# Kernel optimization log

Measured on AMD Instinct MI355X. Metric: run time of the kernel, lower is better.

## Reference

```python
import jax, jax.numpy as jnp
import numpy as np

B, N, D = 4, 4096, 512
E = 4 * D            # expanded_dim = 2048
TAIL = E // 2        # tail_dim = 1024
HALF = TAIL // 2     # mt_half = 512
HEAD = E - TAIL      # head_dim = 1024
EPS_RMS = 1e-6
EPS_NORM = 1e-12


def setup_inputs() -> dict:
    key = jax.random.key(0)
    k = jax.random.split(key, 6)
    x = jax.random.normal(k[0], (B, N, D), dtype=jnp.float32)
    g = jnp.ones((D,), dtype=jnp.float32)                                   # RMSNorm gain
    W1 = jax.random.normal(k[1], (D, E), dtype=jnp.float32) * 0.02          # Enricher linear
    b1 = jnp.zeros((E,), dtype=jnp.float32)
    V = jax.random.normal(k[2], (N, N), dtype=jnp.float32) * 0.02           # learned positional matrix slice
    bias = jnp.zeros((HALF,), dtype=jnp.float32)                            # contextualizer bias
    Wf = jax.random.normal(k[3], (HEAD + HALF, D), dtype=jnp.float32) * 0.02  # Fuser linear (no bias)
    return {"x": x, "g": g, "W1": W1, "b1": b1, "V": V, "bias": bias, "Wf": Wf}


def reference(x, g, W1, b1, V, bias, Wf):
    # RMSNorm
    xn = x * jax.lax.rsqrt(jnp.mean(jnp.square(x), axis=-1, keepdims=True) + EPS_RMS) * g
    # Enricher: relu(linear)^2
    enriched = jnp.square(jax.nn.relu(xn @ W1 + b1))                        # [B, N, E]
    head = enriched[..., :HEAD]                                             # [B, N, HEAD]
    tail = enriched[..., HEAD:]                                             # [B, N, TAIL]
    # Contextualizer
    x_left = tail[..., :HALF]
    x_right = tail[..., HALF:]
    nrm = jnp.sqrt(jnp.sum(jnp.square(x_right), axis=-1, keepdims=True))
    xr_n = x_right / jnp.maximum(nrm, EPS_NORM)                             # F.normalize, p=2
    cos = jnp.einsum('bnd,bmd->bnm', xr_n, xr_n)                            # [B, N, N] cosine sim
    weighted = V[None, :, :] * cos                                          # elementwise learned V
    ctx = jnp.einsum('bnm,bmd->bnd', weighted, xr_n)                        # chunked-path bmm uses x_right_norm
    ctx = jax.nn.sigmoid(ctx + bias)
    gated = x_left * ctx                                                    # [B, N, HALF]
    # Fuser + residual
    out = jnp.concatenate([head, gated], axis=-1) @ Wf                      # [B, N, D]
    return x + out
```

## Files before the change

### kernel.cpp

```cpp
#include <hip/hip_runtime.h>
#include <stdint.h>

typedef unsigned short u16;
typedef unsigned long long u64;
typedef __attribute__((ext_vector_type(8))) short bf16x8;
typedef __attribute__((ext_vector_type(4))) float f32x4;
typedef __attribute__((ext_vector_type(16))) float f32x16;
typedef __attribute__((ext_vector_type(4))) unsigned int u32x4;
typedef __attribute__((ext_vector_type(4))) unsigned short u16x4;

#define DEV static __device__ __forceinline__

DEV u16 f2bf(float f){
  unsigned u = __builtin_bit_cast(unsigned, f);
  u += 0x7fffu + ((u >> 16) & 1u);
  return (u16)(u >> 16);
}
DEV float bf2f(u16 v){
  unsigned u = ((unsigned)v) << 16;
  return __builtin_bit_cast(float, u);
}

DEV void async_lds16(const void* g, void* l){
  __builtin_amdgcn_global_load_lds(
      (const __attribute__((address_space(1))) unsigned int*)g,
      (__attribute__((address_space(3))) unsigned int*)l, 16, 0, 0);
}

DEV f32x4 mfma16(bf16x8 a, bf16x8 b, f32x4 c){
  return __builtin_amdgcn_mfma_f32_16x16x32_bf16(a, b, c, 0, 0, 0);
}
DEV f32x16 mfma32(bf16x8 a, bf16x8 b, f32x16 c){
  return __builtin_amdgcn_mfma_f32_32x32x16_bf16(a, b, c, 0, 0, 0);
}

__global__ __launch_bounds__(64) void k_rms(const float* __restrict__ x,
                                            const float* __restrict__ g,
                                            u16* __restrict__ xn){
  const int row = blockIdx.x;
  const int l = threadIdx.x;
  const float* xr = x + (size_t)row * 512 + l * 8;
  f32x4 a = *(const f32x4*)xr;
  f32x4 c = *(const f32x4*)(xr + 4);
  float s = a[0]*a[0]+a[1]*a[1]+a[2]*a[2]+a[3]*a[3]
          + c[0]*c[0]+c[1]*c[1]+c[2]*c[2]+c[3]*c[3];
  #pragma unroll
  for (int off = 32; off >= 1; off >>= 1) s += __shfl_xor(s, off);
  float sc = rsqrtf(s * (1.f/512.f) + 1e-6f);
  f32x4 g0 = *(const f32x4*)&g[l*8];
  f32x4 g1 = *(const f32x4*)&g[l*8+4];
  u32x4 o;
  o[0] = (unsigned)f2bf(a[0]*sc*g0[0]) | ((unsigned)f2bf(a[1]*sc*g0[1]) << 16);
  o[1] = (unsigned)f2bf(a[2]*sc*g0[2]) | ((unsigned)f2bf(a[3]*sc*g0[3]) << 16);
  o[2] = (unsigned)f2bf(c[0]*sc*g1[0]) | ((unsigned)f2bf(c[1]*sc*g1[1]) << 16);
  o[3] = (unsigned)f2bf(c[2]*sc*g1[2]) | ((unsigned)f2bf(c[3]*sc*g1[3]) << 16);
  *(u32x4*)&xn[(size_t)row*512 + l*8] = o;
}

__global__ __launch_bounds__(64) void k_norm(const float* __restrict__ xr_in,
                                             u16* __restrict__ xrn){
  const int row = blockIdx.x;
  const int l = threadIdx.x;
  const float* xr = xr_in + (size_t)row * 512 + l * 8;
  f32x4 a = *(const f32x4*)xr;
  f32x4 c = *(const f32x4*)(xr + 4);
  float s = a[0]*a[0]+a[1]*a[1]+a[2]*a[2]+a[3]*a[3]
          + c[0]*c[0]+c[1]*c[1]+c[2]*c[2]+c[3]*c[3];
  #pragma unroll
  for (int off = 32; off >= 1; off >>= 1) s += __shfl_xor(s, off);
  float sc = 1.f / fmaxf(sqrtf(s), 1e-12f);
  u32x4 o;
  o[0] = (unsigned)f2bf(a[0]*sc) | ((unsigned)f2bf(a[1]*sc) << 16);
  o[1] = (unsigned)f2bf(a[2]*sc) | ((unsigned)f2bf(a[3]*sc) << 16);
  o[2] = (unsigned)f2bf(c[0]*sc) | ((unsigned)f2bf(c[1]*sc) << 16);
  o[3] = (unsigned)f2bf(c[2]*sc) | ((unsigned)f2bf(c[3]*sc) << 16);
  *(u32x4*)&xrn[(size_t)row*512 + l*8] = o;
}

__global__ __launch_bounds__(256) void k_castV(const float* __restrict__ V,
                                               u16* __restrict__ Vb){
  size_t i = ((size_t)blockIdx.x * 256 + threadIdx.x) * 8;
  f32x4 a = *(const f32x4*)&V[i];
  f32x4 c = *(const f32x4*)&V[i+4];
  u32x4 o;
  o[0] = (unsigned)f2bf(a[0]) | ((unsigned)f2bf(a[1]) << 16);
  o[1] = (unsigned)f2bf(a[2]) | ((unsigned)f2bf(a[3]) << 16);
  o[2] = (unsigned)f2bf(c[0]) | ((unsigned)f2bf(c[1]) << 16);
  o[3] = (unsigned)f2bf(c[2]) | ((unsigned)f2bf(c[3]) << 16);
  *(u32x4*)&Vb[i] = o;
}

__global__ __launch_bounds__(256) void k_tr32(const float* __restrict__ in,
                                              u16* __restrict__ out, int R, int C){
  __shared__ float tile[32][33];
  const int t = threadIdx.x;
  const int r = t >> 3;
  const int c4 = (t & 7) << 2;
  const int r0 = blockIdx.y << 5, c0 = blockIdx.x << 5;
  f32x4 v = *(const f32x4*)&in[(size_t)(r0 + r) * C + c0 + c4];
  tile[r][c4+0]=v[0]; tile[r][c4+1]=v[1]; tile[r][c4+2]=v[2]; tile[r][c4+3]=v[3];
  __syncthreads();
  u64 o =
      (u64)f2bf(tile[c4+0][r])
    | ((u64)f2bf(tile[c4+1][r]) << 16)
    | ((u64)f2bf(tile[c4+2][r]) << 32)
    | ((u64)f2bf(tile[c4+3][r]) << 48);
  *(u64*)&out[(size_t)(c0 + r) * R + r0 + c4] = o;
}

__global__ __launch_bounds__(256) void k_trb(const u16* __restrict__ in,
                                             u16* __restrict__ out, int R, int C){
  __shared__ u16 tile[32][40];
  const int t = threadIdx.x;
  const int r = t >> 3;
  const int c4 = (t & 7) << 2;
  const size_t bb = (size_t)blockIdx.z * R * C;
  const int r0 = blockIdx.y << 5, c0 = blockIdx.x << 5;
  u64 v = *(const u64*)&in[bb + (size_t)(r0 + r)*C + c0 + c4];
  tile[r][c4+0]=(u16)v; tile[r][c4+1]=(u16)(v>>16);
  tile[r][c4+2]=(u16)(v>>32); tile[r][c4+3]=(u16)(v>>48);
  __syncthreads();
  u64 o =
      (u64)tile[c4+0][r]
    | ((u64)tile[c4+1][r] << 16)
    | ((u64)tile[c4+2][r] << 32)
    | ((u64)tile[c4+3][r] << 48);
  *(u64*)&out[bb + (size_t)(c0 + r) * R + r0 + c4] = o;
}

__global__ __launch_bounds__(256) void k_gemm1(const u16* __restrict__ A,
                                               const u16* __restrict__ Bt,
                                               const float* __restrict__ b1,
                                               u16* __restrict__ head,
                                               float* __restrict__ xleft,
                                               float* __restrict__ xright){
  __shared__ u16 As[128*32];
  __shared__ u16 Bs[128*32];
  const int t = threadIdx.x;
  const int l = t & 63;
  const int w = t >> 6;
  const int wr = w >> 1, wc = w & 1;
  const int m0 = blockIdx.x << 7;
  const int n0 = blockIdx.y << 7;
  const int ra = t >> 2;
  const int kb = (t & 3) << 3;
  const int lr = l & 15, lh = l >> 4;
  f32x4 acc[4][4];
  #pragma unroll
  for (int i=0;i<4;i++)
    #pragma unroll
    for (int j=0;j<4;j++)
      #pragma unroll
      for (int r=0;r<4;r++) acc[i][j][r] = 0.f;
  for (int k0 = 0; k0 < 512; k0 += 32){
    async_lds16(A  + (size_t)(m0 + ra)*512      + k0 + kb, &As[t*8]);
    async_lds16(A  + (size_t)(m0 + 64 + ra)*512 + k0 + kb, &As[2048 + t*8]);
    async_lds16(Bt + (size_t)(n0 + ra)*512      + k0 + kb, &Bs[t*8]);
    async_lds16(Bt + (size_t)(n0 + 64 + ra)*512 + k0 + kb, &Bs[2048 + t*8]);
    __syncthreads();
    bf16x8 af[4], bfr[4];
    #pragma unroll
    for (int i=0;i<4;i++){
      af[i]  = *(const bf16x8*)&As[(wr*64 + i*16 + lr)*32 + lh*8];
      bfr[i] = *(const bf16x8*)&Bs[(wc*64 + i*16 + lr)*32 + lh*8];
    }
    #pragma unroll
    for (int i=0;i<4;i++)
      #pragma unroll
      for (int j=0;j<4;j++)
        acc[i][j] = mfma16(af[i], bfr[j], acc[i][j]);
    __syncthreads();
  }
  #pragma unroll
  for (int i=0;i<4;i++){
    #pragma unroll
    for (int j=0;j<4;j++){
      int c = n0 + wc*64 + j*16 + lr;
      float bb = b1[c];
      #pragma unroll
      for (int r=0;r<4;r++){
        int m = m0 + wr*64 + i*16 + lh*4 + r;
        float v = acc[i][j][r] + bb;
        v = v > 0.f ? v*v : 0.f;
        if (c < 1024)      head[(size_t)m*1024 + c] = f2bf(v);
        else if (c < 1536) xleft[(size_t)m*512 + (c - 1024)] = v;
        else               xright[(size_t)m*512 + (c - 1536)] = v;
      }
    }
  }
}

__global__ __launch_bounds__(256) void k_gemm3(const u16* __restrict__ head,
                                               const u16* __restrict__ gated,
                                               const u16* __restrict__ Wft,
                                               const float* __restrict__ x,
                                               float* __restrict__ out){
  __shared__ u16 As[128*32];
  __shared__ u16 Bs[128*32];
  const int t = threadIdx.x;
  const int l = t & 63;
  const int w = t >> 6;
  const int wr = w >> 1, wc = w & 1;
  const int m0 = blockIdx.x << 7;
  const int n0 = blockIdx.y << 7;
  const int ra = t >> 2;
  const int kb = (t & 3) << 3;
  const int lr = l & 15, lh = l >> 4;
  f32x4 acc[4][4];
  #pragma unroll
  for (int i=0;i<4;i++)
    #pragma unroll
    for (int j=0;j<4;j++)
      #pragma unroll
      for (int r=0;r<4;r++) acc[i][j][r] = 0.f;
  for (int k0 = 0; k0 < 1536; k0 += 32){
    const u16* sa; size_t lda; int kk;
    if (k0 < 1024){ sa = head;  lda = 1024; kk = k0; }
    else          { sa = gated; lda = 512;  kk = k0 - 1024; }
    async_lds16(sa + (size_t)(m0 + ra)*lda      + kk + kb, &As[t*8]);
    async_lds16(sa + (size_t)(m0 + 64 + ra)*lda + kk + kb, &As[2048 + t*8]);
    async_lds16(Wft + (size_t)(n0 + ra)*1536      + k0 + kb, &Bs[t*8]);
    async_lds16(Wft + (size_t)(n0 + 64 + ra)*1536 + k0 + kb, &Bs[2048 + t*8]);
    __syncthreads();
    bf16x8 af[4], bfr[4];
    #pragma unroll
    for (int i=0;i<4;i++){
      af[i]  = *(const bf16x8*)&As[(wr*64 + i*16 + lr)*32 + lh*8];
      bfr[i] = *(const bf16x8*)&Bs[(wc*64 + i*16 + lr)*32 + lh*8];
    }
    #pragma unroll
    for (int i=0;i<4;i++)
      #pragma unroll
      for (int j=0;j<4;j++)
        acc[i][j] = mfma16(af[i], bfr[j], acc[i][j]);
    __syncthreads();
  }
  #pragma unroll
  for (int i=0;i<4;i++){
    #pragma unroll
    for (int j=0;j<4;j++){
      int c = n0 + wc*64 + j*16 + lr;
      #pragma unroll
      for (int r=0;r<4;r++){
        int m = m0 + wr*64 + i*16 + lh*4 + r;
        size_t gi = (size_t)m*512 + c;
        out[gi] = x[gi] + acc[i][j][r];
      }
    }
  }
}

__global__ __launch_bounds__(512, 2) void k_attn(const u16* __restrict__ xrn,
                                                 const u16* __restrict__ xrT,
                                                 const u16* __restrict__ Vb,
                                                 const float* __restrict__ bias,
                                                 const float* __restrict__ xleft,
                                                 u16* __restrict__ gated){
  __shared__ char smem[154624];
  char* km = smem;
  char* tt = smem + 65536;
  char* ps = smem + 131072;
  char* pb = smem + 149504;
  const int t = threadIdx.x;
  const int l = t & 63, w = t >> 6;
  const int wr = w >> 2, ks = w & 3, wc = (w >> 1) & 1, kq2 = w & 1;
  const int lo = l & 31, hi = l >> 5;
  const int bid = blockIdx.x;
  const int b  = (bid & 7) >> 1;
  const int n0 = ((((bid >> 3) << 1) | (bid & 1))) << 6;
  const u16* xb  = xrn + (size_t)b * (4096*512);
  const u16* xTb = xrT + (size_t)b * (512*4096);

  bf16x8 areg[8];
  {
    const u16* apt = xb + (size_t)(n0 + wr*32 + lo)*512 + ks*128 + hi*8;
    #pragma unroll
    for (int kq = 0; kq < 8; ++kq) areg[kq] = *(const bf16x8*)(apt + kq*16);
  }
  f32x16 acc[8];
  #pragma unroll
  for (int i = 0; i < 8; ++i)
    #pragma unroll
    for (int j = 0; j < 16; ++j) acc[i][j] = 0.f;

  const int prf = t >> 3;
  const int pc4 = (t & 7) << 2;
  const int wrr = prf >> 5, prr = prf & 31;

  #pragma unroll
  for (int c = 0; c < 4; ++c){
    int off = (c*512 + t)*16;
    int row = off >> 10, colb = off & 1023;
    async_lds16(xb + (size_t)row*512 + ((colb ^ ((row&7)<<4)) >> 1), km + off);
    int dr = off >> 6, cb2 = off & 63;
    async_lds16(xTb + (size_t)dr*4096 + ((cb2 ^ ((dr&6)<<3)) >> 1), tt + off);
  }
  __syncthreads();

  int cur = 0;
  for (int it = 0; it < 128; ++it){
    const int m0 = it << 5;
    u16x4 vv = *(const u16x4*)&Vb[(size_t)(n0 + prf)*4096 + m0 + pc4];
    if (it < 127){
      const int m1 = m0 + 32;
      const int nb = (cur ^ 1) * 32768;
      #pragma unroll
      for (int c = 0; c < 4; ++c){
        int off = (c*512 + t)*16;
        int row = off >> 10, colb = off & 1023;
        async_lds16(xb + (size_t)(m1 + row)*512 + ((colb ^ ((row&7)<<4)) >> 1),
                    km + nb + off);
        int dr = off >> 6, cb2 = off & 63;
        async_lds16(xTb + (size_t)dr*4096 + m1 + ((cb2 ^ ((dr&6)<<3)) >> 1),
                    tt + nb + off);
      }
    }
    f32x16 S0, S1;
    #pragma unroll
    for (int j = 0; j < 16; ++j){ S0[j] = 0.f; S1[j] = 0.f; }
    {
      const char* kbp = km + cur*32768 + lo*1024;
      const int swk = (lo & 7) << 4;
      #pragma unroll
      for (int kq = 0; kq < 8; kq += 2){
        bf16x8 b0 = *(const bf16x8*)(kbp + ((ks*256 + kq*32 + hi*16) ^ swk));
        bf16x8 b1 = *(const bf16x8*)(kbp + ((ks*256 + (kq+1)*32 + hi*16) ^ swk));
        S0 = mfma32(areg[kq],   b0, S0);
        S1 = mfma32(areg[kq+1], b1, S1);
      }
    }
    {
      char* pw = ps + ((wr*4 + ks)*32)*72 + lo*2;
      #pragma unroll
      for (int rg = 0; rg < 16; ++rg){
        int prow = (rg & 3) + 8*(rg >> 2) + 4*hi;
        *(u16*)(pw + prow*72) = f2bf(S0[rg] + S1[rg]);
      }
    }
    asm volatile("s_waitcnt lgkmcnt(0)" ::: "memory");
    __builtin_amdgcn_s_barrier();
    __builtin_amdgcn_sched_barrier(0);
    {
      float s0=0.f, s1=0.f, s2=0.f, s3=0.f;
      #pragma unroll
      for (int k2 = 0; k2 < 4; ++k2){
        u16x4 pv = *(const u16x4*)(ps + (((wrr*4 + k2)*32 + prr)*36 + pc4)*2);
        s0 += bf2f(pv[0]); s1 += bf2f(pv[1]); s2 += bf2f(pv[2]); s3 += bf2f(pv[3]);
      }
      u64 po = (u64)f2bf(s0 * bf2f(vv[0]))
             | ((u64)f2bf(s1 * bf2f(vv[1])) << 16)
             | ((u64)f2bf(s2 * bf2f(vv[2])) << 32)
             | ((u64)f2bf(s3 * bf2f(vv[3])) << 48);
      *(u64*)(pb + (prf*40 + pc4)*2) = po;
    }
    asm volatile("s_waitcnt lgkmcnt(0)" ::: "memory");
    __builtin_amdgcn_s_barrier();
    __builtin_amdgcn_sched_barrier(0);
    {
      bf16x8 pa = *(const bf16x8*)(pb + (wr*32 + lo)*80 + kq2*32 + hi*16);
      const char* tb = tt + cur*32768;
      #pragma unroll
      for (int ds = 0; ds < 8; ++ds){
        int drow = wc*256 + ds*32 + lo;
        bf16x8 bfr = *(const bf16x8*)(tb + drow*64 +
                       ((kq2*32 + hi*16) ^ ((drow & 6) << 3)));
        acc[ds] = mfma32(pa, bfr, acc[ds]);
      }
    }
    __syncthreads();
    cur ^= 1;
  }

  float* red = (float*)smem;
  const int rbase = (wr*2 + wc) * 8192;
  if (kq2 == 1){
    #pragma unroll
    for (int ds = 0; ds < 8; ++ds)
      #pragma unroll
      for (int rg = 0; rg < 16; ++rg)
        red[rbase + (ds*16 + rg)*64 + l] = acc[ds][rg];
  }
  __syncthreads();
  if (kq2 == 0){
    #pragma unroll
    for (int ds = 0; ds < 8; ++ds){
      const int d = wc*256 + ds*32 + lo;
      const float bs = bias[d];
      #pragma unroll
      for (int rg = 0; rg < 16; ++rg){
        int row = n0 + wr*32 + (rg & 3) + 8*(rg >> 2) + 4*hi;
        float v = acc[ds][rg] + red[rbase + (ds*16 + rg)*64 + l] + bs;
        v = 1.f / (1.f + __expf(-v));
        size_t gi = (size_t)(b*4096 + row)*512 + d;
        gated[gi] = f2bf(xleft[gi] * v);
      }
    }
  }
}

extern "C" void kernel_launch(void* const* d_in, const int* in_sizes, int n_in,
                              void* d_out, int out_size, void* d_ws, size_t ws_size,
                              hipStream_t stream){
  const float* x    = (const float*)d_in[0];
  const float* g    = (const float*)d_in[1];
  const float* W1   = (const float*)d_in[2];
  const float* b1   = (const float*)d_in[3];
  const float* V    = (const float*)d_in[4];
  const float* bias = (const float*)d_in[5];
  const float* Wf   = (const float*)d_in[6];
  float* out = (float*)d_out;

  char* ws = (char*)d_ws;
  const size_t MB = 1024u*1024u;
  u16*   xn     = (u16*)  (ws + 0*MB);
  u16*   W1t    = (u16*)  (ws + 16*MB);
  u16*   Vbf    = (u16*)  (ws + 0*MB);
  u16*   Wft    = (u16*)  (ws + 32*MB);
  u16*   head   = (u16*)  (ws + 34*MB);
  float* xleft  = (float*)(ws + 66*MB);
  float* xright = (float*)(ws + 98*MB);
  u16*   gated  = (u16*)  (ws + 98*MB);
  u16*   xrn    = (u16*)  (ws + 130*MB);
  u16*   xrT    = (u16*)  (ws + 146*MB);

  k_rms  <<<dim3(16384),      dim3(64),  0, stream>>>(x, g, xn);
  k_tr32 <<<dim3(64, 16),     dim3(256), 0, stream>>>(W1, W1t, 512, 2048);
  k_tr32 <<<dim3(16, 48),     dim3(256), 0, stream>>>(Wf, Wft, 1536, 512);
  k_gemm1<<<dim3(128, 16),    dim3(256), 0, stream>>>(xn, W1t, b1, head, xleft, xright);
  k_castV<<<dim3(8192),       dim3(256), 0, stream>>>(V, Vbf);
  k_norm <<<dim3(16384),      dim3(64),  0, stream>>>(xright, xrn);
  k_trb  <<<dim3(16, 128, 4), dim3(256), 0, stream>>>(xrn, xrT, 4096, 512);
  k_attn <<<dim3(256),        dim3(512), 0, stream>>>(xrn, xrT, Vbf, bias, xleft, gated);
  k_gemm3<<<dim3(128, 4),     dim3(256), 0, stream>>>(head, gated, Wft, x, out);
}
```

Baseline: 390.9 us.

## Halve attention block tile to 32 rows, drop double buffering, add setprio

The attention kernel now uses 256-thread blocks over 32 query rows instead of 512 threads over 64 rows, and launches 512 blocks, so the LDS footprint halves and more blocks fit per CU. The double-buffered async prefetch is replaced by a single buffer loaded at the top of each iteration behind barriers. The transposed-key tile gets a new swizzle layout, and s_setprio brackets the MFMA sections. The trade-off is more overlap from higher occupancy against doubled K/V global traffic per output row and less latency hiding inside each block.

```diff
diff --git a/kernel.cpp b/kernel.cpp
--- a/kernel.cpp
+++ b/kernel.cpp
@@ -250,30 +250,30 @@
   }
 }
 
-__global__ __launch_bounds__(512, 2) void k_attn(const u16* __restrict__ xrn,
+__global__ __launch_bounds__(256, 2) void k_attn(const u16* __restrict__ xrn,
                                                  const u16* __restrict__ xrT,
                                                  const u16* __restrict__ Vb,
                                                  const float* __restrict__ bias,
                                                  const float* __restrict__ xleft,
                                                  u16* __restrict__ gated){
-  __shared__ char smem[154624];
+  __shared__ char smem[77312];
   char* km = smem;
-  char* tt = smem + 65536;
-  char* ps = smem + 131072;
-  char* pb = smem + 149504;
+  char* tq = smem + 32768;
+  char* ps = smem + 65536;
+  char* pb = smem + 74752;
   const int t = threadIdx.x;
   const int l = t & 63, w = t >> 6;
-  const int wr = w >> 2, ks = w & 3, wc = (w >> 1) & 1, kq2 = w & 1;
+  const int ks = w, wd = w >> 1, kq2 = w & 1;
   const int lo = l & 31, hi = l >> 5;
   const int bid = blockIdx.x;
   const int b  = (bid & 7) >> 1;
-  const int n0 = ((((bid >> 3) << 1) | (bid & 1))) << 6;
+  const int n0 = (((bid >> 3) << 1) | (bid & 1)) << 5;
   const u16* xb  = xrn + (size_t)b * (4096*512);
   const u16* xTb = xrT + (size_t)b * (512*4096);
 
   bf16x8 areg[8];
   {
-    const u16* apt = xb + (size_t)(n0 + wr*32 + lo)*512 + ks*128 + hi*8;
+    const u16* apt = xb + (size_t)(n0 + lo)*512 + ks*128 + hi*8;
     #pragma unroll
     for (int kq = 0; kq < 8; ++kq) areg[kq] = *(const bf16x8*)(apt + kq*16);
   }
@@ -285,42 +285,36 @@
 
   const int prf = t >> 3;
   const int pc4 = (t & 7) << 2;
-  const int wrr = prf >> 5, prr = prf & 31;
-
-  #pragma unroll
-  for (int c = 0; c < 4; ++c){
-    int off = (c*512 + t)*16;
-    int row = off >> 10, colb = off & 1023;
-    async_lds16(xb + (size_t)row*512 + ((colb ^ ((row&7)<<4)) >> 1), km + off);
-    int dr = off >> 6, cb2 = off & 63;
-    async_lds16(xTb + (size_t)dr*4096 + ((cb2 ^ ((dr&6)<<3)) >> 1), tt + off);
-  }
-  __syncthreads();
-
-  int cur = 0;
+
   for (int it = 0; it < 128; ++it){
     const int m0 = it << 5;
+    __syncthreads();
     u16x4 vv = *(const u16x4*)&Vb[(size_t)(n0 + prf)*4096 + m0 + pc4];
-    if (it < 127){
-      const int m1 = m0 + 32;
-      const int nb = (cur ^ 1) * 32768;
-      #pragma unroll
-      for (int c = 0; c < 4; ++c){
-        int off = (c*512 + t)*16;
-        int row = off >> 10, colb = off & 1023;
-        async_lds16(xb + (size_t)(m1 + row)*512 + ((colb ^ ((row&7)<<4)) >> 1),
-                    km + nb + off);
-        int dr = off >> 6, cb2 = off & 63;
-        async_lds16(xTb + (size_t)dr*4096 + m1 + ((cb2 ^ ((dr&6)<<3)) >> 1),
-                    tt + nb + off);
-      }
-    }
+    #pragma unroll
+    for (int c = 0; c < 8; ++c){
+      int off = (c*256 + t)*16;
+      int row = off >> 10;
+      int lg  = (off & 1023) ^ ((row & 15) << 4);
+      async_lds16(xb + (size_t)(m0 + row)*512 + (lg >> 1), km + off);
+    }
+    #pragma unroll
+    for (int c = 0; c < 8; ++c){
+      int off = (c*256 + t)*16;
+      int r   = off >> 8;
+      int lg  = (off & 255) ^ ((r & 15) << 4);
+      int q   = lg >> 6;
+      int mc  = (lg & 63) >> 1;
+      async_lds16(xTb + (size_t)(q*128 + r)*4096 + m0 + mc, tq + off);
+    }
+    __syncthreads();
+
     f32x16 S0, S1;
     #pragma unroll
     for (int j = 0; j < 16; ++j){ S0[j] = 0.f; S1[j] = 0.f; }
     {
-      const char* kbp = km + cur*32768 + lo*1024;
-      const int swk = (lo & 7) << 4;
+      const char* kbp = km + lo*1024;
+      const int swk = (lo & 15) << 4;
+      __builtin_amdgcn_s_setprio(1);
       #pragma unroll
       for (int kq = 0; kq < 8; kq += 2){
         bf16x8 b0 = *(const bf16x8*)(kbp + ((ks*256 + kq*32 + hi*16) ^ swk));
@@ -328,9 +322,10 @@
         S0 = mfma32(areg[kq],   b0, S0);
         S1 = mfma32(areg[kq+1], b1, S1);
       }
+      __builtin_amdgcn_s_setprio(0);
     }
     {
-      char* pw = ps + ((wr*4 + ks)*32)*72 + lo*2;
+      char* pw = ps + (ks*32)*72 + lo*2;
       #pragma unroll
       for (int rg = 0; rg < 16; ++rg){
         int prow = (rg & 3) + 8*(rg >> 2) + 4*hi;
@@ -344,7 +339,7 @@
       float s0=0.f, s1=0.f, s2=0.f, s3=0.f;
       #pragma unroll
       for (int k2 = 0; k2 < 4; ++k2){
-        u16x4 pv = *(const u16x4*)(ps + (((wrr*4 + k2)*32 + prr)*36 + pc4)*2);
+        u16x4 pv = *(const u16x4*)(ps + ((k2*32 + prf)*36 + pc4)*2);
         s0 += bf2f(pv[0]); s1 += bf2f(pv[1]); s2 += bf2f(pv[2]); s3 += bf2f(pv[3]);
       }
       u64 po = (u64)f2bf(s0 * bf2f(vv[0]))
@@ -357,41 +352,45 @@
     __builtin_amdgcn_s_barrier();
     __builtin_amdgcn_sched_barrier(0);
     {
-      bf16x8 pa = *(const bf16x8*)(pb + (wr*32 + lo)*80 + kq2*32 + hi*16);
-      const char* tb = tt + cur*32768;
+      bf16x8 pa = *(const bf16x8*)(pb + lo*80 + kq2*32 + hi*16);
+      __builtin_amdgcn_s_setprio(1);
       #pragma unroll
       for (int ds = 0; ds < 8; ++ds){
-        int drow = wc*256 + ds*32 + lo;
-        bf16x8 bfr = *(const bf16x8*)(tb + drow*64 +
-                       ((kq2*32 + hi*16) ^ ((drow & 6) << 3)));
+        int d = wd*256 + ds*32 + lo;
+        int r = d & 127, q = d >> 7;
+        bf16x8 bfr = *(const bf16x8*)(tq + r*256 +
+                       ((q*64 + kq2*32 + hi*16) ^ ((r & 15) << 4)));
         acc[ds] = mfma32(pa, bfr, acc[ds]);
       }
-    }
-    __syncthreads();
-    cur ^= 1;
-  }
-
+      __builtin_amdgcn_s_setprio(0);
+    }
+  }
+
+  __syncthreads();
   float* red = (float*)smem;
-  const int rbase = (wr*2 + wc) * 8192;
   if (kq2 == 1){
     #pragma unroll
-    for (int ds = 0; ds < 8; ++ds)
-      #pragma unroll
-      for (int rg = 0; rg < 16; ++rg)
-        red[rbase + (ds*16 + rg)*64 + l] = acc[ds][rg];
+    for (int ds = 0; ds < 8; ++ds){
+      const int d = wd*256 + ds*32 + lo;
+      #pragma unroll
+      for (int rg = 0; rg < 16; ++rg){
+        int n = (rg & 3) + 8*(rg >> 2) + 4*hi;
+        red[n*512 + d] = acc[ds][rg];
+      }
+    }
   }
   __syncthreads();
   if (kq2 == 0){
     #pragma unroll
     for (int ds = 0; ds < 8; ++ds){
-      const int d = wc*256 + ds*32 + lo;
+      const int d = wd*256 + ds*32 + lo;
       const float bs = bias[d];
       #pragma unroll
       for (int rg = 0; rg < 16; ++rg){
-        int row = n0 + wr*32 + (rg & 3) + 8*(rg >> 2) + 4*hi;
-        float v = acc[ds][rg] + red[rbase + (ds*16 + rg)*64 + l] + bs;
+        int n = (rg & 3) + 8*(rg >> 2) + 4*hi;
+        float v = acc[ds][rg] + red[n*512 + d] + bs;
         v = 1.f / (1.f + __expf(-v));
-        size_t gi = (size_t)(b*4096 + row)*512 + d;
+        size_t gi = (size_t)(b*4096 + n0 + n)*512 + d;
         gated[gi] = f2bf(xleft[gi] * v);
       }
     }
@@ -430,6 +429,6 @@
   k_castV<<<dim3(8192),       dim3(256), 0, stream>>>(V, Vbf);
   k_norm <<<dim3(16384),      dim3(64),  0, stream>>>(xright, xrn);
   k_trb  <<<dim3(16, 128, 4), dim3(256), 0, stream>>>(xrn, xrT, 4096, 512);
-  k_attn <<<dim3(256),        dim3(512), 0, stream>>>(xrn, xrT, Vbf, bias, xleft, gated);
+  k_attn <<<dim3(512),        dim3(256), 0, stream>>>(xrn, xrT, Vbf, bias, xleft, gated);
   k_gemm3<<<dim3(128, 4),     dim3(256), 0, stream>>>(head, gated, Wft, x, out);
 }
```

New measurement: 583.2 us. +49.2%, slower.

## Re-swizzle LDS tiles for attention kernel and add MFMA priority hints

Applied to the files above, without the earlier changes.

The transposed value tile in LDS moves to a 256-byte row layout that packs four 128-row groups and uses an XOR swizzle over 16 rows. The key tile swizzle also widens from 8 to 16 rows, and the P buffer row pitch shrinks from 80 to 72 bytes, which lowers the shared memory footprint. The aim is fewer LDS bank conflicts on the MFMA operand reads. Both MFMA loops are wrapped in s_setprio, and the float-to-bf16 conversion now uses the HIP intrinsic, whose handling of NaN may differ slightly from the old hand-written rounding.

```diff
diff --git a/kernel.cpp b/kernel.cpp
--- a/kernel.cpp
+++ b/kernel.cpp
@@ -1,4 +1,5 @@
 #include <hip/hip_runtime.h>
+#include <hip/hip_bf16.h>
 #include <stdint.h>
 
 typedef unsigned short u16;
@@ -12,9 +13,8 @@
 #define DEV static __device__ __forceinline__
 
 DEV u16 f2bf(float f){
-  unsigned u = __builtin_bit_cast(unsigned, f);
-  u += 0x7fffu + ((u >> 16) & 1u);
-  return (u16)(u >> 16);
+  __hip_bfloat16 h = __float2bfloat16(f);
+  return __builtin_bit_cast(u16, h);
 }
 DEV float bf2f(u16 v){
   unsigned u = ((unsigned)v) << 16;
@@ -256,9 +256,9 @@
                                                  const float* __restrict__ bias,
                                                  const float* __restrict__ xleft,
                                                  u16* __restrict__ gated){
-  __shared__ char smem[154624];
+  __shared__ char smem[153600];
   char* km = smem;
-  char* tt = smem + 65536;
+  char* tq = smem + 65536;
   char* ps = smem + 131072;
   char* pb = smem + 149504;
   const int t = threadIdx.x;
@@ -291,9 +291,12 @@
   for (int c = 0; c < 4; ++c){
     int off = (c*512 + t)*16;
     int row = off >> 10, colb = off & 1023;
-    async_lds16(xb + (size_t)row*512 + ((colb ^ ((row&7)<<4)) >> 1), km + off);
-    int dr = off >> 6, cb2 = off & 63;
-    async_lds16(xTb + (size_t)dr*4096 + ((cb2 ^ ((dr&6)<<3)) >> 1), tt + off);
+    async_lds16(xb + (size_t)row*512 + ((colb ^ ((row&15)<<4)) >> 1), km + off);
+    int r   = off >> 8;
+    int lg  = (off & 255) ^ ((r & 15) << 4);
+    int q   = lg >> 6;
+    int mc  = (lg & 63) >> 1;
+    async_lds16(xTb + (size_t)(q*128 + r)*4096 + mc, tq + off);
   }
   __syncthreads();
 
@@ -308,11 +311,13 @@
       for (int c = 0; c < 4; ++c){
         int off = (c*512 + t)*16;
         int row = off >> 10, colb = off & 1023;
-        async_lds16(xb + (size_t)(m1 + row)*512 + ((colb ^ ((row&7)<<4)) >> 1),
+        async_lds16(xb + (size_t)(m1 + row)*512 + ((colb ^ ((row&15)<<4)) >> 1),
                     km + nb + off);
-        int dr = off >> 6, cb2 = off & 63;
-        async_lds16(xTb + (size_t)dr*4096 + m1 + ((cb2 ^ ((dr&6)<<3)) >> 1),
-                    tt + nb + off);
+        int r   = off >> 8;
+        int lg  = (off & 255) ^ ((r & 15) << 4);
+        int q   = lg >> 6;
+        int mc  = (lg & 63) >> 1;
+        async_lds16(xTb + (size_t)(q*128 + r)*4096 + m1 + mc, tq + nb + off);
       }
     }
     f32x16 S0, S1;
@@ -320,7 +325,8 @@
     for (int j = 0; j < 16; ++j){ S0[j] = 0.f; S1[j] = 0.f; }
     {
       const char* kbp = km + cur*32768 + lo*1024;
-      const int swk = (lo & 7) << 4;
+      const int swk = (lo & 15) << 4;
+      __builtin_amdgcn_s_setprio(1);
       #pragma unroll
       for (int kq = 0; kq < 8; kq += 2){
         bf16x8 b0 = *(const bf16x8*)(kbp + ((ks*256 + kq*32 + hi*16) ^ swk));
@@ -328,6 +334,7 @@
         S0 = mfma32(areg[kq],   b0, S0);
         S1 = mfma32(areg[kq+1], b1, S1);
       }
+      __builtin_amdgcn_s_setprio(0);
     }
     {
       char* pw = ps + ((wr*4 + ks)*32)*72 + lo*2;
@@ -351,21 +358,24 @@
              | ((u64)f2bf(s1 * bf2f(vv[1])) << 16)
              | ((u64)f2bf(s2 * bf2f(vv[2])) << 32)
              | ((u64)f2bf(s3 * bf2f(vv[3])) << 48);
-      *(u64*)(pb + (prf*40 + pc4)*2) = po;
+      *(u64*)(pb + prf*72 + pc4*2) = po;
     }
     asm volatile("s_waitcnt lgkmcnt(0)" ::: "memory");
     __builtin_amdgcn_s_barrier();
     __builtin_amdgcn_sched_barrier(0);
     {
-      bf16x8 pa = *(const bf16x8*)(pb + (wr*32 + lo)*80 + kq2*32 + hi*16);
-      const char* tb = tt + cur*32768;
+      bf16x8 pa = *(const bf16x8*)(pb + (wr*32 + lo)*72 + kq2*32 + hi*16);
+      const char* tb = tq + cur*32768;
+      __builtin_amdgcn_s_setprio(1);
       #pragma unroll
       for (int ds = 0; ds < 8; ++ds){
-        int drow = wc*256 + ds*32 + lo;
-        bf16x8 bfr = *(const bf16x8*)(tb + drow*64 +
-                       ((kq2*32 + hi*16) ^ ((drow & 6) << 3)));
+        int d = wc*256 + ds*32 + lo;
+        int r = d & 127, q = d >> 7;
+        bf16x8 bfr = *(const bf16x8*)(tb + r*256 +
+                       ((q*64 + kq2*32 + hi*16) ^ ((r & 15) << 4)));
         acc[ds] = mfma32(pa, bfr, acc[ds]);
       }
+      __builtin_amdgcn_s_setprio(0);
     }
     __syncthreads();
     cur ^= 1;
```

New measurement: 426.0 us. +9.0%, slower.
